# Performance work log

Hardware: AMD Instinct MI355X
Metric: run time of the kernel (lower is better)

Reference implementation:

```python
import jax, jax.numpy as jnp
import numpy as np

N_NODES = 50000
N_EDGES = 800000


def _graph_conv(feature, W, b, src, dst, edge_w, n_nodes, activation=None):
    # DGL GraphConv, norm='both', with edge_weight.
    ones = jnp.ones((src.shape[0],), dtype=feature.dtype)
    deg_out = jnp.clip(jax.ops.segment_sum(ones, src, num_segments=n_nodes), 1.0)
    deg_in = jnp.clip(jax.ops.segment_sum(ones, dst, num_segments=n_nodes), 1.0)
    # scale src side by out-deg^-1/2, transform first (in_feats > out_feats path)
    h = (feature * (deg_out ** -0.5)[:, None]) @ W            # [N, out]
    msgs = h[src] * edge_w[:, None]                            # [E, out]
    agg = jax.ops.segment_sum(msgs, dst, num_segments=n_nodes) # [N, out]
    out = agg * (deg_in ** -0.5)[:, None] + b
    if activation is not None:
        out = activation(out)
    return out


def setup_inputs() -> dict:
    key = jax.random.key(0)
    ks = jax.random.split(key, 8)
    feature = jax.random.normal(ks[0], (N_NODES, 768), dtype=jnp.float32)
    src = jax.random.randint(ks[1], (N_EDGES,), 0, N_NODES, dtype=jnp.int32)
    dst = jax.random.randint(ks[2], (N_EDGES,), 0, N_NODES, dtype=jnp.int32)
    edge_w = jax.random.uniform(ks[3], (N_EDGES,), dtype=jnp.float32)
    W1 = jax.random.normal(ks[4], (768, 200), dtype=jnp.float32) * (768 ** -0.5)
    b1 = jnp.zeros((200,), dtype=jnp.float32)
    W2 = jax.random.normal(ks[5], (200, 20), dtype=jnp.float32) * (200 ** -0.5)
    b2 = jnp.zeros((20,), dtype=jnp.float32)
    return {"feature": feature, "src": src, "dst": dst, "edge_w": edge_w,
            "W1": W1, "b1": b1, "W2": W2, "b2": b2}


def reference(feature, src, dst, edge_w, W1, b1, W2, b2):
    n = feature.shape[0]
    # dropout layers are identity in eval mode
    h = _graph_conv(feature, W1, b1, src, dst, edge_w, n, activation=jax.nn.relu)
    out = _graph_conv(h, W2, b2, src, dst, edge_w, n)
    return out
```

## Files before the change

kernel.cpp:

```cpp
#include <hip/hip_runtime.h>

#define N_NODES 50000
#define N_EDGES 800000
#define F_IN 768
#define H1 200
#define H2 20
#define NB_SCAN 196

typedef unsigned short ushort_t;
typedef __attribute__((ext_vector_type(8))) short bf16x8;
typedef __attribute__((ext_vector_type(4))) float f32x4;


__global__ __launch_bounds__(256) void k_count(const int* __restrict__ src,
                                               const int* __restrict__ dst,
                                               int* __restrict__ cnt_src,
                                               int* __restrict__ cnt_dst) {
  int i = blockIdx.x * 256 + threadIdx.x;
  if (i < N_EDGES) {
    atomicAdd(&cnt_src[src[i]], 1);
    atomicAdd(&cnt_dst[dst[i]], 1);
  }
}

__global__ __launch_bounds__(256) void k_scan_block(const int* __restrict__ cnt_dst,
                                                    int* __restrict__ row_start,
                                                    int* __restrict__ partials) {
  __shared__ int sm[256];
  int i = blockIdx.x * 256 + threadIdx.x;
  int v = (i < N_NODES) ? cnt_dst[i] : 0;
  sm[threadIdx.x] = v;
  __syncthreads();
#pragma unroll
  for (int off = 1; off < 256; off <<= 1) {
    int t = (threadIdx.x >= off) ? sm[threadIdx.x - off] : 0;
    __syncthreads();
    sm[threadIdx.x] += t;
    __syncthreads();
  }
  if (i < N_NODES) row_start[i] = sm[threadIdx.x] - v;
  if (threadIdx.x == 255) partials[blockIdx.x] = sm[255];
}

__global__ __launch_bounds__(256) void k_scan_partials(int* __restrict__ partials) {
  __shared__ int sm[256];
  int v = (threadIdx.x < NB_SCAN) ? partials[threadIdx.x] : 0;
  sm[threadIdx.x] = v;
  __syncthreads();
#pragma unroll
  for (int off = 1; off < 256; off <<= 1) {
    int t = (threadIdx.x >= off) ? sm[threadIdx.x - off] : 0;
    __syncthreads();
    sm[threadIdx.x] += t;
    __syncthreads();
  }
  partials[threadIdx.x] = sm[threadIdx.x] - v;
}

__global__ __launch_bounds__(256) void k_scan_add(const int* __restrict__ cnt_dst,
                                                  const int* __restrict__ cnt_src,
                                                  const int* __restrict__ partials,
                                                  int* __restrict__ row_start,
                                                  float* __restrict__ dinv_in,
                                                  float* __restrict__ dinv_out) {
  int i = blockIdx.x * 256 + threadIdx.x;
  if (i < N_NODES) {
    row_start[i] += partials[blockIdx.x];
    dinv_in[i] = rsqrtf(fmaxf((float)cnt_dst[i], 1.f));
    dinv_out[i] = rsqrtf(fmaxf((float)cnt_src[i], 1.f));
  }
}

__global__ __launch_bounds__(256) void k_fill(const int* __restrict__ src,
                                              const int* __restrict__ dst,
                                              const float* __restrict__ ew,
                                              const int* __restrict__ row_start,
                                              int* __restrict__ cursor,
                                              int* __restrict__ src_s,
                                              float* __restrict__ w_s) {
  int e = blockIdx.x * 256 + threadIdx.x;
  if (e < N_EDGES) {
    int d = dst[e];
    int pos = atomicAdd(&cursor[d], 1);
    int idx = row_start[d] + pos;
    src_s[idx] = src[e];
    w_s[idx] = ew[e];
  }
}

__global__ __launch_bounds__(256) void k_splitW(const float* __restrict__ W1,
                                                ushort_t* __restrict__ WH,
                                                ushort_t* __restrict__ WL) {
  int idx = blockIdx.x * 256 + threadIdx.x;
  if (idx >= 208 * F_IN) return;
  int col = idx / F_IN, k = idx % F_IN;
  float f = (col < H1) ? W1[k * H1 + col] : 0.f;
  unsigned b = __float_as_uint(f);
  unsigned h = b >> 16;
  float lo = f - __uint_as_float(h << 16);
  WH[idx] = (ushort_t)h;
  WL[idx] = (ushort_t)(__float_as_uint(lo) >> 16);
}

#define NT 13

__global__ __launch_bounds__(256) void k_gemm1_mfma(
    const float* __restrict__ A,
    const ushort_t* __restrict__ BH,
    const ushort_t* __restrict__ BL,
    const float* __restrict__ dinv_out,
    float* __restrict__ H) {
  __shared__ ushort_t AsH[64][32];
  __shared__ ushort_t AsL[64][32];
  __shared__ ushort_t BsH[NT][16][32];
  __shared__ ushort_t BsL[NT][16][32];

  const int t = threadIdx.x;
  const int wid = t >> 6;
  const int lane = t & 63;
  const int bm = blockIdx.x * 64;
  const int arow = t >> 2;
  const int akq = (t & 3) * 8;
  const int frow = lane & 15;
  const int fkq = (lane >> 4) * 8;

  f32x4 acc[NT];
#pragma unroll
  for (int i = 0; i < NT; ++i) acc[i] = (f32x4)(0.f);

  const int agr = bm + arow;
  const float* __restrict__ arowp = &A[(size_t)agr * F_IN + akq];

  for (int k0 = 0; k0 < F_IN; k0 += 32) {
    float4 v0 = make_float4(0.f, 0.f, 0.f, 0.f), v1 = v0;
    if (agr < N_NODES) {
      v0 = *(const float4*)&arowp[k0];
      v1 = *(const float4*)&arowp[k0 + 4];
    }
    float fv[8] = {v0.x, v0.y, v0.z, v0.w, v1.x, v1.y, v1.z, v1.w};
    unsigned hp[4], lp[4];
#pragma unroll
    for (int i = 0; i < 4; ++i) {
      unsigned b0 = __float_as_uint(fv[2 * i]);
      unsigned b1 = __float_as_uint(fv[2 * i + 1]);
      unsigned h0 = b0 >> 16, h1 = b1 >> 16;
      float lo0 = fv[2 * i] - __uint_as_float(h0 << 16);
      float lo1 = fv[2 * i + 1] - __uint_as_float(h1 << 16);
      hp[i] = h0 | (h1 << 16);
      lp[i] = (__float_as_uint(lo0) >> 16) | (__float_as_uint(lo1) & 0xffff0000u);
    }

    __syncthreads();

    *(uint4*)&AsH[arow][akq] = make_uint4(hp[0], hp[1], hp[2], hp[3]);
    *(uint4*)&AsL[arow][akq] = make_uint4(lp[0], lp[1], lp[2], lp[3]);

    {
      int bcol = lane >> 2;
      int bko = (lane & 3) * 8;
      for (int nt = wid; nt < NT; nt += 4) {
        const ushort_t* gh = &BH[(size_t)(nt * 16 + bcol) * F_IN + k0 + bko];
        const ushort_t* gl = &BL[(size_t)(nt * 16 + bcol) * F_IN + k0 + bko];
        __builtin_amdgcn_global_load_lds(gh, &BsH[nt][0][0], 16, 0, 0);
        __builtin_amdgcn_global_load_lds(gl, &BsL[nt][0][0], 16, 0, 0);
      }
    }

    __syncthreads();

    bf16x8 aH = *(const bf16x8*)&AsH[wid * 16 + frow][fkq];
    bf16x8 aL = *(const bf16x8*)&AsL[wid * 16 + frow][fkq];
#pragma unroll
    for (int nt = 0; nt < NT; ++nt) {
      bf16x8 bH = *(const bf16x8*)&BsH[nt][frow][fkq];
      bf16x8 bL = *(const bf16x8*)&BsL[nt][frow][fkq];
      acc[nt] = __builtin_amdgcn_mfma_f32_16x16x32_bf16(aH, bH, acc[nt], 0, 0, 0);
      acc[nt] = __builtin_amdgcn_mfma_f32_16x16x32_bf16(aH, bL, acc[nt], 0, 0, 0);
      acc[nt] = __builtin_amdgcn_mfma_f32_16x16x32_bf16(aL, bH, acc[nt], 0, 0, 0);
    }
  }

  const int r0 = bm + wid * 16 + (lane >> 4) * 4;
  float dsc[4];
#pragma unroll
  for (int r = 0; r < 4; ++r)
    dsc[r] = (r0 + r < N_NODES) ? dinv_out[r0 + r] : 0.f;
#pragma unroll
  for (int nt = 0; nt < NT; ++nt) {
    int gc = nt * 16 + (lane & 15);
    if (gc < H1) {
#pragma unroll
      for (int r = 0; r < 4; ++r) {
        int gr = r0 + r;
        if (gr < N_NODES) H[(size_t)gr * H1 + gc] = acc[nt][r] * dsc[r];
      }
    }
  }
}

__global__ __launch_bounds__(256) void k_layer1(
    const int* __restrict__ row_start, const int* __restrict__ cnt,
    const int* __restrict__ src_s, const float* __restrict__ w_s,
    const float* __restrict__ H, const float* __restrict__ dinv_in,
    const float* __restrict__ dinv_out, const float* __restrict__ b1,
    const float* __restrict__ W2, float* __restrict__ G) {
  __shared__ float Tsm[4][H1];
  const int wid = threadIdx.x >> 6;
  const int lane = threadIdx.x & 63;
  const int node = __builtin_amdgcn_readfirstlane(blockIdx.x * 4 + wid);
  const int start = __builtin_amdgcn_readfirstlane(row_start[node]);
  const int n = __builtin_amdgcn_readfirstlane(cnt[node]);
  const float4* __restrict__ Hv = (const float4*)H;
  const bool act = lane < (H1 / 4);
  float4 acc = make_float4(0.f, 0.f, 0.f, 0.f);

  int e = 0;
  for (; e + 2 <= n; e += 2) {
    int s0 = src_s[start + e];
    int s1 = src_s[start + e + 1];
    float w0 = w_s[start + e];
    float w1 = w_s[start + e + 1];
    if (act) {
      float4 v0 = Hv[s0 * (H1 / 4) + lane];
      float4 v1 = Hv[s1 * (H1 / 4) + lane];
      acc.x = fmaf(w0, v0.x, acc.x);
      acc.y = fmaf(w0, v0.y, acc.y);
      acc.z = fmaf(w0, v0.z, acc.z);
      acc.w = fmaf(w0, v0.w, acc.w);
      acc.x = fmaf(w1, v1.x, acc.x);
      acc.y = fmaf(w1, v1.y, acc.y);
      acc.z = fmaf(w1, v1.z, acc.z);
      acc.w = fmaf(w1, v1.w, acc.w);
    }
  }
  if (e < n) {
    int s0 = src_s[start + e];
    float w0 = w_s[start + e];
    if (act) {
      float4 v0 = Hv[s0 * (H1 / 4) + lane];
      acc.x = fmaf(w0, v0.x, acc.x);
      acc.y = fmaf(w0, v0.y, acc.y);
      acc.z = fmaf(w0, v0.z, acc.z);
      acc.w = fmaf(w0, v0.w, acc.w);
    }
  }

  if (act) {
    float di = dinv_in[node];
    float dn = dinv_out[node];
    float4 bb = ((const float4*)b1)[lane];
    float4 r;
    r.x = fmaxf(fmaf(acc.x, di, bb.x), 0.f) * dn;
    r.y = fmaxf(fmaf(acc.y, di, bb.y), 0.f) * dn;
    r.z = fmaxf(fmaf(acc.z, di, bb.z), 0.f) * dn;
    r.w = fmaxf(fmaf(acc.w, di, bb.w), 0.f) * dn;
    *(float4*)&Tsm[wid][lane * 4] = r;
  }
  __syncthreads();

  if (lane < H2) {
    float a = 0.f;
#pragma unroll 8
    for (int d = 0; d < H1; ++d) a = fmaf(Tsm[wid][d], W2[d * H2 + lane], a);
    G[node * H2 + lane] = a;
  }
}

__global__ __launch_bounds__(256) void k_agg2_final(
    const int* __restrict__ row_start, const int* __restrict__ cnt,
    const int* __restrict__ src_s, const float* __restrict__ w_s,
    const float* __restrict__ G, const float* __restrict__ dinv_in,
    const float* __restrict__ b2, float* __restrict__ out) {
  int gi = blockIdx.x * 256 + threadIdx.x;
  if (gi >= N_NODES * H2) return;
  int node = gi / H2;
  int dim = gi % H2;
  int start = row_start[node];
  int n = cnt[node];
  float acc = 0.f;
  int e = 0;
  for (; e + 2 <= n; e += 2) {
    int s0 = src_s[start + e];
    int s1 = src_s[start + e + 1];
    float w0 = w_s[start + e];
    float w1 = w_s[start + e + 1];
    float g0 = G[s0 * H2 + dim];
    float g1 = G[s1 * H2 + dim];
    acc = fmaf(w0, g0, acc);
    acc = fmaf(w1, g1, acc);
  }
  if (e < n) {
    int s0 = src_s[start + e];
    acc = fmaf(w_s[start + e], G[s0 * H2 + dim], acc);
  }
  out[gi] = fmaf(acc, dinv_in[node], b2[dim]);
}

extern "C" void kernel_launch(void* const* d_in, const int* in_sizes, int n_in,
                              void* d_out, int out_size, void* d_ws, size_t ws_size,
                              hipStream_t stream) {
  const float* feature = (const float*)d_in[0];
  const int* src = (const int*)d_in[1];
  const int* dst = (const int*)d_in[2];
  const float* edge_w = (const float*)d_in[3];
  const float* W1 = (const float*)d_in[4];
  const float* b1 = (const float*)d_in[5];
  const float* W2 = (const float*)d_in[6];
  const float* b2 = (const float*)d_in[7];
  float* out = (float*)d_out;

  char* wsb = (char*)d_ws;
  int* cnt_dst = (int*)(wsb + 0);
  int* cnt_src = (int*)(wsb + 200000);
  int* cursor = (int*)(wsb + 400000);
  int* partials = (int*)(wsb + 600000);
  int* row_start = (int*)(wsb + 601024);
  float* dinv_in = (float*)(wsb + 801024);
  float* dinv_out = (float*)(wsb + 1001024);
  int* src_s = (int*)(wsb + 1201024);
  float* w_s = (float*)(wsb + 4401024);
  float* h = (float*)(wsb + 7601024);
  float* g2 = (float*)(wsb + 47601024);
  ushort_t* W1sH = (ushort_t*)(wsb + 51601024);
  ushort_t* W1sL = (ushort_t*)(wsb + 51920512);

  hipMemsetAsync(wsb, 0, 600000, stream);

  k_count<<<(N_EDGES + 255) / 256, 256, 0, stream>>>(src, dst, cnt_src, cnt_dst);
  k_scan_block<<<NB_SCAN, 256, 0, stream>>>(cnt_dst, row_start, partials);
  k_scan_partials<<<1, 256, 0, stream>>>(partials);
  k_scan_add<<<NB_SCAN, 256, 0, stream>>>(cnt_dst, cnt_src, partials, row_start,
                                          dinv_in, dinv_out);
  k_fill<<<(N_EDGES + 255) / 256, 256, 0, stream>>>(src, dst, edge_w, row_start,
                                                    cursor, src_s, w_s);
  k_splitW<<<(208 * F_IN + 255) / 256, 256, 0, stream>>>(W1, W1sH, W1sL);

  k_gemm1_mfma<<<(N_NODES + 63) / 64, 256, 0, stream>>>(feature, W1sH, W1sL,
                                                        dinv_out, h);

  k_layer1<<<N_NODES / 4, 256, 0, stream>>>(row_start, cnt_dst, src_s, w_s, h,
                                            dinv_in, dinv_out, b1, W2, g2);
  k_agg2_final<<<(N_NODES * H2 + 255) / 256, 256, 0, stream>>>(
      row_start, cnt_dst, src_s, w_s, g2, dinv_in, b2, out);
}
```

Baseline: 580.4 us.

## Retile GEMM1 to 32-row blocks with 2x2 warp split, swizzled LDS, A prefetch

The first-layer MFMA GEMM now processes 32 rows per block instead of 64. The four waves are split 2x2 over rows and N-tiles (7+6 tiles each), which raises the block count and shrinks the per-wave accumulators. LDS A and B tiles get an XOR-style slot swizzle to cut bank conflicts, and the next A chunk is prefetched into registers before the barrier to overlap the global load with the MFMAs. H is stored with a padded 208-float row stride so the aggregation gathers stay aligned, at the cost of more B traffic per output row and a slightly larger workspace.

```diff
diff --git a/kernel.cpp b/kernel.cpp
--- a/kernel.cpp
+++ b/kernel.cpp
@@ -4,8 +4,10 @@
 #define N_EDGES 800000
 #define F_IN 768
 #define H1 200
+#define H1P 208
 #define H2 20
 #define NB_SCAN 196
+#define NT 13
 
 typedef unsigned short ushort_t;
 typedef __attribute__((ext_vector_type(8))) short bf16x8;
@@ -102,41 +104,53 @@
   WL[idx] = (ushort_t)(__float_as_uint(lo) >> 16);
 }
 
-#define NT 13
-
 __global__ __launch_bounds__(256) void k_gemm1_mfma(
     const float* __restrict__ A,
     const ushort_t* __restrict__ BH,
     const ushort_t* __restrict__ BL,
     const float* __restrict__ dinv_out,
     float* __restrict__ H) {
-  __shared__ ushort_t AsH[64][32];
-  __shared__ ushort_t AsL[64][32];
+  __shared__ ushort_t AsH[32][32];
+  __shared__ ushort_t AsL[32][32];
   __shared__ ushort_t BsH[NT][16][32];
   __shared__ ushort_t BsL[NT][16][32];
 
   const int t = threadIdx.x;
   const int wid = t >> 6;
   const int lane = t & 63;
-  const int bm = blockIdx.x * 64;
+  const int bm = blockIdx.x * 32;
+
+  const bool astage = t < 128;
   const int arow = t >> 2;
-  const int akq = (t & 3) * 8;
+  const int akq = t & 3;
+  const int aslot = (akq + ((arow >> 1) & 3)) & 3;
+  const int agr = bm + arow;
+  const float* __restrict__ arowp = &A[(size_t)agr * F_IN + akq * 8];
+
   const int frow = lane & 15;
-  const int fkq = (lane >> 4) * 8;
-
-  f32x4 acc[NT];
-#pragma unroll
-  for (int i = 0; i < NT; ++i) acc[i] = (f32x4)(0.f);
-
-  const int agr = bm + arow;
-  const float* __restrict__ arowp = &A[(size_t)agr * F_IN + akq];
+  const int kq = lane >> 4;
+  const int wm = wid & 1;
+  const int wn = wid >> 1;
+  const int ntbase = wn * 7;
+  const int ntcnt = wn ? 6 : 7;
+  const int row_local = wm * 16 + frow;
+  const int arslot = (kq + ((row_local >> 1) & 3)) & 3;
+  const int brslot = (kq + ((frow >> 1) & 3)) & 3;
+
+  const int bf = lane >> 2;
+  const int bq = ((lane & 3) - ((lane >> 3) & 3)) & 3;
+
+  f32x4 acc[7];
+#pragma unroll
+  for (int i = 0; i < 7; ++i) acc[i] = (f32x4)(0.f);
+
+  float4 v0 = make_float4(0.f, 0.f, 0.f, 0.f), v1 = v0;
+  if (astage && agr < N_NODES) {
+    v0 = *(const float4*)&arowp[0];
+    v1 = *(const float4*)&arowp[4];
+  }
 
   for (int k0 = 0; k0 < F_IN; k0 += 32) {
-    float4 v0 = make_float4(0.f, 0.f, 0.f, 0.f), v1 = v0;
-    if (agr < N_NODES) {
-      v0 = *(const float4*)&arowp[k0];
-      v1 = *(const float4*)&arowp[k0 + 4];
-    }
     float fv[8] = {v0.x, v0.y, v0.z, v0.w, v1.x, v1.y, v1.z, v1.w};
     unsigned hp[4], lp[4];
 #pragma unroll
@@ -152,48 +166,54 @@
 
     __syncthreads();
 
-    *(uint4*)&AsH[arow][akq] = make_uint4(hp[0], hp[1], hp[2], hp[3]);
-    *(uint4*)&AsL[arow][akq] = make_uint4(lp[0], lp[1], lp[2], lp[3]);
-
-    {
-      int bcol = lane >> 2;
-      int bko = (lane & 3) * 8;
-      for (int nt = wid; nt < NT; nt += 4) {
-        const ushort_t* gh = &BH[(size_t)(nt * 16 + bcol) * F_IN + k0 + bko];
-        const ushort_t* gl = &BL[(size_t)(nt * 16 + bcol) * F_IN + k0 + bko];
-        __builtin_amdgcn_global_load_lds(gh, &BsH[nt][0][0], 16, 0, 0);
-        __builtin_amdgcn_global_load_lds(gl, &BsL[nt][0][0], 16, 0, 0);
-      }
-    }
-
-    __syncthreads();
-
-    bf16x8 aH = *(const bf16x8*)&AsH[wid * 16 + frow][fkq];
-    bf16x8 aL = *(const bf16x8*)&AsL[wid * 16 + frow][fkq];
-#pragma unroll
-    for (int nt = 0; nt < NT; ++nt) {
-      bf16x8 bH = *(const bf16x8*)&BsH[nt][frow][fkq];
-      bf16x8 bL = *(const bf16x8*)&BsL[nt][frow][fkq];
-      acc[nt] = __builtin_amdgcn_mfma_f32_16x16x32_bf16(aH, bH, acc[nt], 0, 0, 0);
-      acc[nt] = __builtin_amdgcn_mfma_f32_16x16x32_bf16(aH, bL, acc[nt], 0, 0, 0);
-      acc[nt] = __builtin_amdgcn_mfma_f32_16x16x32_bf16(aL, bH, acc[nt], 0, 0, 0);
-    }
-  }
-
-  const int r0 = bm + wid * 16 + (lane >> 4) * 4;
+    if (astage) {
+      *(uint4*)&AsH[arow][aslot * 8] = make_uint4(hp[0], hp[1], hp[2], hp[3]);
+      *(uint4*)&AsL[arow][aslot * 8] = make_uint4(lp[0], lp[1], lp[2], lp[3]);
+    }
+
+    for (int nt = wid; nt < NT; nt += 4) {
+      const ushort_t* gh = &BH[(size_t)(nt * 16 + bf) * F_IN + k0 + bq * 8];
+      const ushort_t* gl = &BL[(size_t)(nt * 16 + bf) * F_IN + k0 + bq * 8];
+      __builtin_amdgcn_global_load_lds(gh, &BsH[nt][0][0], 16, 0, 0);
+      __builtin_amdgcn_global_load_lds(gl, &BsL[nt][0][0], 16, 0, 0);
+    }
+
+    v0 = make_float4(0.f, 0.f, 0.f, 0.f);
+    v1 = v0;
+    if (k0 + 32 < F_IN && astage && agr < N_NODES) {
+      v0 = *(const float4*)&arowp[k0 + 32];
+      v1 = *(const float4*)&arowp[k0 + 36];
+    }
+
+    __syncthreads();
+
+    bf16x8 aH = *(const bf16x8*)&AsH[row_local][arslot * 8];
+    bf16x8 aL = *(const bf16x8*)&AsL[row_local][arslot * 8];
+#pragma unroll
+    for (int i = 0; i < 7; ++i) {
+      if (i >= ntcnt) break;
+      int nt = ntbase + i;
+      bf16x8 bH = *(const bf16x8*)&BsH[nt][frow][brslot * 8];
+      bf16x8 bL = *(const bf16x8*)&BsL[nt][frow][brslot * 8];
+      acc[i] = __builtin_amdgcn_mfma_f32_16x16x32_bf16(aH, bH, acc[i], 0, 0, 0);
+      acc[i] = __builtin_amdgcn_mfma_f32_16x16x32_bf16(aH, bL, acc[i], 0, 0, 0);
+      acc[i] = __builtin_amdgcn_mfma_f32_16x16x32_bf16(aL, bH, acc[i], 0, 0, 0);
+    }
+  }
+
+  const int r0 = bm + wm * 16 + kq * 4;
   float dsc[4];
 #pragma unroll
   for (int r = 0; r < 4; ++r)
     dsc[r] = (r0 + r < N_NODES) ? dinv_out[r0 + r] : 0.f;
 #pragma unroll
-  for (int nt = 0; nt < NT; ++nt) {
-    int gc = nt * 16 + (lane & 15);
-    if (gc < H1) {
-#pragma unroll
-      for (int r = 0; r < 4; ++r) {
-        int gr = r0 + r;
-        if (gr < N_NODES) H[(size_t)gr * H1 + gc] = acc[nt][r] * dsc[r];
-      }
+  for (int i = 0; i < 7; ++i) {
+    if (i >= ntcnt) break;
+    int gc = (ntbase + i) * 16 + frow;
+#pragma unroll
+    for (int r = 0; r < 4; ++r) {
+      int gr = r0 + r;
+      if (gr < N_NODES) H[(size_t)gr * H1P + gc] = acc[i][r] * dsc[r];
     }
   }
 }
@@ -221,27 +241,27 @@
     float w0 = w_s[start + e];
     float w1 = w_s[start + e + 1];
     if (act) {
-      float4 v0 = Hv[s0 * (H1 / 4) + lane];
-      float4 v1 = Hv[s1 * (H1 / 4) + lane];
-      acc.x = fmaf(w0, v0.x, acc.x);
-      acc.y = fmaf(w0, v0.y, acc.y);
-      acc.z = fmaf(w0, v0.z, acc.z);
-      acc.w = fmaf(w0, v0.w, acc.w);
-      acc.x = fmaf(w1, v1.x, acc.x);
-      acc.y = fmaf(w1, v1.y, acc.y);
-      acc.z = fmaf(w1, v1.z, acc.z);
-      acc.w = fmaf(w1, v1.w, acc.w);
+      float4 u0 = Hv[(size_t)s0 * (H1P / 4) + lane];
+      float4 u1 = Hv[(size_t)s1 * (H1P / 4) + lane];
+      acc.x = fmaf(w0, u0.x, acc.x);
+      acc.y = fmaf(w0, u0.y, acc.y);
+      acc.z = fmaf(w0, u0.z, acc.z);
+      acc.w = fmaf(w0, u0.w, acc.w);
+      acc.x = fmaf(w1, u1.x, acc.x);
+      acc.y = fmaf(w1, u1.y, acc.y);
+      acc.z = fmaf(w1, u1.z, acc.z);
+      acc.w = fmaf(w1, u1.w, acc.w);
     }
   }
   if (e < n) {
     int s0 = src_s[start + e];
     float w0 = w_s[start + e];
     if (act) {
-      float4 v0 = Hv[s0 * (H1 / 4) + lane];
-      acc.x = fmaf(w0, v0.x, acc.x);
-      acc.y = fmaf(w0, v0.y, acc.y);
-      acc.z = fmaf(w0, v0.z, acc.z);
-      acc.w = fmaf(w0, v0.w, acc.w);
+      float4 u0 = Hv[(size_t)s0 * (H1P / 4) + lane];
+      acc.x = fmaf(w0, u0.x, acc.x);
+      acc.y = fmaf(w0, u0.y, acc.y);
+      acc.z = fmaf(w0, u0.z, acc.z);
+      acc.w = fmaf(w0, u0.w, acc.w);
     }
   }
 
@@ -320,9 +340,9 @@
   int* src_s = (int*)(wsb + 1201024);
   float* w_s = (float*)(wsb + 4401024);
   float* h = (float*)(wsb + 7601024);
-  float* g2 = (float*)(wsb + 47601024);
-  ushort_t* W1sH = (ushort_t*)(wsb + 51601024);
-  ushort_t* W1sL = (ushort_t*)(wsb + 51920512);
+  float* g2 = (float*)(wsb + 49201024);
+  ushort_t* W1sH = (ushort_t*)(wsb + 53201024);
+  ushort_t* W1sL = (ushort_t*)(wsb + 53520512);
 
   hipMemsetAsync(wsb, 0, 600000, stream);
 
@@ -335,7 +355,7 @@
                                                     cursor, src_s, w_s);
   k_splitW<<<(208 * F_IN + 255) / 256, 256, 0, stream>>>(W1, W1sH, W1sL);
 
-  k_gemm1_mfma<<<(N_NODES + 63) / 64, 256, 0, stream>>>(feature, W1sH, W1sL,
+  k_gemm1_mfma<<<(N_NODES + 31) / 32, 256, 0, stream>>>(feature, W1sH, W1sL,
                                                         dinv_out, h);
 
   k_layer1<<<N_NODES / 4, 256, 0, stream>>>(row_start, cnt_dst, src_s, w_s, h,
```

Result: slower. 604.4 us (+4.1%).
